# Optimization experiments

Hardware: AMD Instinct MI355X
Metric: run time of the kernel (lower is better)

## Reference

```python
import jax, jax.numpy as jnp
import numpy as np

N = 100_000   # nodes
E = 1_600_000 # edges (avg degree 16)
D = 128       # feature dim (input = hidden = output = mlp hidden)
L = 3         # GIN layers
EPS = 0.0     # init_eps, not learned


def setup_inputs() -> dict:
    key = jax.random.key(0)
    ks = jax.random.split(key, 7)
    feat = jax.random.normal(ks[0], (N, D), jnp.float32)
    # scale weights ~ 1/sqrt(fan_in) for numerically sane activations
    W1 = jax.random.normal(ks[1], (L, D, D), jnp.float32) / np.float32(np.sqrt(D))
    b1 = jax.random.normal(ks[2], (L, D), jnp.float32) * 0.01
    W2 = jax.random.normal(ks[3], (L, D, D), jnp.float32) / np.float32(np.sqrt(D))
    b2 = jax.random.normal(ks[4], (L, D), jnp.float32) * 0.01
    src = jax.random.randint(ks[5], (E,), 0, N, dtype=jnp.int32)
    dst = jax.random.randint(ks[6], (E,), 0, N, dtype=jnp.int32)
    return {"feat": feat, "W1": W1, "b1": b1, "W2": W2, "b2": b2,
            "src": src, "dst": dst}


def reference(feat, W1, b1, W2, b2, src, dst):
    h = feat
    for i in range(L):
        # sum-aggregate neighbor (source) features into destination nodes
        neigh = jax.ops.segment_sum(h[src], dst, num_segments=N)  # [N, D]
        rst = (1.0 + EPS) * h + neigh
        # 2-layer MLP: hidden layer uses act+norm(none), last layer is plain linear
        if i < L - 1:
            h1 = jax.nn.relu(rst @ W1[i] + b1[i])
            h2 = h1 @ W2[i] + b2[i]
            h = jax.nn.relu(h2)  # ApplyNodeFunc: norm(none) -> relu
        else:
            # last GIN layer: activation 'none' everywhere
            h1 = rst @ W1[i] + b1[i]
            h = h1 @ W2[i] + b2[i]
    return h
```

## Files before the change

kernel.cpp:

```cpp
#include <hip/hip_runtime.h>
#include <hip/hip_bf16.h>

#define D 128
#define NBUCK_SHIFT 9
#define PAD_SLACK 2048

typedef __bf16 bf16x8 __attribute__((ext_vector_type(8)));
typedef float f32x4 __attribute__((ext_vector_type(4)));
typedef float f32x2 __attribute__((ext_vector_type(2)));
typedef int i32x4 __attribute__((ext_vector_type(4)));
typedef int i32x2 __attribute__((ext_vector_type(2)));
typedef unsigned int u32x4 __attribute__((ext_vector_type(4)));
typedef unsigned short u16x4_t __attribute__((ext_vector_type(4)));
typedef unsigned short u16x8_t __attribute__((ext_vector_type(8)));

__device__ __forceinline__ unsigned short f2b(float f) {
    __hip_bfloat16 h = __float2bfloat16(f);
    return __builtin_bit_cast(unsigned short, h);
}

__device__ __forceinline__ void acc8(f32x2* acc, u32x4 x) {
#pragma unroll
    for (int r = 0; r < 4; ++r) {
        f32x2 t;
        t[0] = __builtin_bit_cast(float, x[r] << 16);
        t[1] = __builtin_bit_cast(float, x[r] & 0xffff0000u);
        acc[r] += t;
    }
}

__global__ __launch_bounds__(256) void coarse_hist_kernel(
        const int* __restrict__ dst, int* __restrict__ bco, int E, int nbuck) {
    __shared__ int s[256];
    int t = threadIdx.x;
    s[t] = 0;
    __syncthreads();
    for (int i = blockIdx.x * 256 + t; i < E; i += gridDim.x * 256)
        atomicAdd(&s[dst[i] >> NBUCK_SHIFT], 1);
    __syncthreads();
    if (t < nbuck && s[t] > 0) atomicAdd(&bco[t], s[t]);
}

__global__ __launch_bounds__(256) void bucket_scan_kernel(
        const int* __restrict__ bco, int* __restrict__ bbase, int nbuck, int E) {
    __shared__ int s[256];
    int t = threadIdx.x;
    int c = (t < nbuck) ? bco[t] : 0;
    s[t] = c;
    __syncthreads();
    for (int o = 1; o < 256; o <<= 1) {
        int y = (t >= o) ? s[t - o] : 0;
        __syncthreads();
        s[t] += y;
        __syncthreads();
    }
    if (t < nbuck) bbase[t] = s[t] - c;
    if (t == 0) bbase[nbuck] = E;
}

__global__ __launch_bounds__(256) void bucket_kernel(
        const int* __restrict__ src, const int* __restrict__ dst,
        const int* __restrict__ bbase, int* __restrict__ bcursor,
        unsigned int* __restrict__ pairs, int E, int nbuck) {
    __shared__ int lcnt[256];
    __shared__ int lbase[256];
    int t = threadIdx.x;
    int base = blockIdx.x * 4096;
    if (t < nbuck) lcnt[t] = 0;
    __syncthreads();
    int d[16], s[16];
#pragma unroll
    for (int k = 0; k < 16; ++k) {
        int i = base + t + k * 256;
        if (i < E) {
            d[k] = dst[i];
            s[k] = src[i];
            atomicAdd(&lcnt[d[k] >> NBUCK_SHIFT], 1);
        } else {
            d[k] = -1;
            s[k] = 0;
        }
    }
    __syncthreads();
    if (t < nbuck) {
        int c = lcnt[t];
        int g = (c > 0) ? atomicAdd(&bcursor[t], c) : 0;
        lbase[t] = bbase[t] + g;
        lcnt[t] = 0;
    }
    __syncthreads();
#pragma unroll
    for (int k = 0; k < 16; ++k) {
        if (d[k] >= 0) {
            int b = d[k] >> NBUCK_SHIFT;
            int r = atomicAdd(&lcnt[b], 1);
            pairs[lbase[b] + r] = ((unsigned)s[k] << 9) | ((unsigned)d[k] & 511u);
        }
    }
}

__global__ __launch_bounds__(1024) void bucket_build_kernel(
        const unsigned int* __restrict__ pairs, const int* __restrict__ bbase,
        i32x2* __restrict__ rowse, int* __restrict__ col, int* __restrict__ rowhead,
        int N, int E) {
    __shared__ int cnt[512];
    __shared__ int off[512];
    int t = threadIdx.x;
    int b = blockIdx.x;
    int s0 = bbase[b], s1 = bbase[b + 1];
    int p0 = ((s0 + 3) & ~3) + b * PAD_SLACK;
    if (t < 512) cnt[t] = 0;
    __syncthreads();
    for (int i = s0 + t; i < s1; i += 1024)
        atomicAdd(&cnt[pairs[i] & 511u], 1);
    __syncthreads();
    int deg = (t < 512) ? cnt[t] : 0;
    int ovp = (deg > 15) ? ((deg - 15 + 3) & ~3) : 0;
    if (t < 512) off[t] = ovp;
    __syncthreads();
    for (int o = 1; o < 512; o <<= 1) {
        int y = (t < 512 && t >= o) ? off[t - o] : 0;
        __syncthreads();
        if (t < 512) off[t] += y;
        __syncthreads();
    }
    int v0 = b << NBUCK_SHIFT;
    int zoff = N << 8;
    if (t < 512) {
        int ex = off[t] - ovp;
        off[t] = ex;
        cnt[t] = 0;
        int v = v0 + t;
        if (v < N) {
            i32x2 se;
            se[0] = p0 + ex;
            se[1] = p0 + ex + ovp;
            rowse[v] = se;
            int* rhv = rowhead + (size_t)v * 16;
            rhv[0] = v << 8;
            int ninl = deg < 15 ? deg : 15;
            for (int q = 1 + ninl; q < 16; ++q) rhv[q] = zoff;
        }
    }
    __syncthreads();
    for (int i = s0 + t; i < s1; i += 1024) {
        unsigned int p = pairs[i];
        int li = (int)(p & 511u);
        int x = (int)(p >> 9);
        int s = atomicAdd(&cnt[li], 1);
        if (s < 15) rowhead[(size_t)(v0 + li) * 16 + 1 + s] = x << 8;
        else        col[p0 + off[li] + (s - 15)] = x << 8;
    }
    __syncthreads();
    if (t < 512) {
        int cc = cnt[t];
        int ovreal = (cc > 15) ? cc - 15 : 0;
        int base2 = p0 + off[t];
        int endp = base2 + ((ovreal + 3) & ~3);
        for (int q = base2 + ovreal; q < endp; ++q) col[q] = zoff;
    }
}

__global__ void f32_to_bf16_kernel(const float4* __restrict__ in, ushort4* __restrict__ out, int n4) {
    int i = blockIdx.x * blockDim.x + threadIdx.x;
    if (i < n4) {
        float4 f = in[i];
        ushort4 o;
        o.x = f2b(f.x); o.y = f2b(f.y); o.z = f2b(f.z); o.w = f2b(f.w);
        out[i] = o;
    }
}

__global__ void wtrans_kernel(const float* __restrict__ W1, const float* __restrict__ W2,
                              unsigned short* __restrict__ W1L, unsigned short* __restrict__ W2L,
                              int total) {
    int i = blockIdx.x * blockDim.x + threadIdx.x;
    if (i < total) {
        int l = i >> 14;
        int rem = i & 16383;
        int k = rem >> 7;
        int n = rem & 127;
        int nt = n >> 4, l15 = n & 15;
        int kb = k >> 5, lg = (k >> 3) & 3, j = k & 7;
        int o = ((l * 32 + nt * 4 + kb) * 64 + lg * 16 + l15) * 8 + j;
        W1L[o] = f2b(W1[i]);
        W2L[o] = f2b(W2[i]);
    }
}

__global__ __launch_bounds__(256) void agg_kernel(
        const unsigned short* __restrict__ h, const i32x2* __restrict__ rowse,
        const int* __restrict__ col, const i32x4* __restrict__ rowhead,
        unsigned short* __restrict__ rst, int N) {
    int lane = threadIdx.x & 63;
    int i = lane & 15;
    int j = lane >> 4;
    int v = blockIdx.x * 4 + (threadIdx.x >> 6);
    if (v >= N) return;

    const char* __restrict__ hb = (const char*)h;
    unsigned ioff = (unsigned)i * 16u;

    i32x4 c4 = __builtin_nontemporal_load(&rowhead[(size_t)v * 4 + j]);
    i32x2 se = __builtin_nontemporal_load(&rowse[v]);

    f32x2 accA[4], accB[4], accC[4], accD[4];
#pragma unroll
    for (int r = 0; r < 4; ++r) {
        accA[r] = (f32x2){0.f, 0.f};
        accB[r] = (f32x2){0.f, 0.f};
        accC[r] = (f32x2){0.f, 0.f};
        accD[r] = (f32x2){0.f, 0.f};
    }

    u32x4 x0 = *(const u32x4*)(hb + ((unsigned)c4[0] + ioff));
    u32x4 x1 = *(const u32x4*)(hb + ((unsigned)c4[1] + ioff));
    u32x4 x2 = *(const u32x4*)(hb + ((unsigned)c4[2] + ioff));
    u32x4 x3 = *(const u32x4*)(hb + ((unsigned)c4[3] + ioff));

    int e = se[0] + 4 * j;
    int e1 = se[1];
    bool have = (e < e1);
    i32x4 o4;
    if (have) o4 = __builtin_nontemporal_load((const i32x4*)(col + e));

    acc8(accA, x0);
    acc8(accB, x1);
    acc8(accC, x2);
    acc8(accD, x3);

    while (have) {
        int en = e + 16;
        bool haven = (en < e1);
        i32x4 o4n;
        if (haven) o4n = __builtin_nontemporal_load((const i32x4*)(col + en));
        u32x4 y0 = *(const u32x4*)(hb + ((unsigned)o4[0] + ioff));
        u32x4 y1 = *(const u32x4*)(hb + ((unsigned)o4[1] + ioff));
        u32x4 y2 = *(const u32x4*)(hb + ((unsigned)o4[2] + ioff));
        u32x4 y3 = *(const u32x4*)(hb + ((unsigned)o4[3] + ioff));
        acc8(accA, y0);
        acc8(accB, y1);
        acc8(accC, y2);
        acc8(accD, y3);
        o4 = o4n;
        e = en;
        have = haven;
    }

    unsigned short outv[8];
#pragma unroll
    for (int r = 0; r < 4; ++r) {
        f32x2 s = (accA[r] + accB[r]) + (accC[r] + accD[r]);
        float lo = s[0], hi = s[1];
        lo += __shfl_xor(lo, 16);
        lo += __shfl_xor(lo, 32);
        hi += __shfl_xor(hi, 16);
        hi += __shfl_xor(hi, 32);
        outv[2 * r] = f2b(lo);
        outv[2 * r + 1] = f2b(hi);
    }
    if (j == 0) {
        u16x8_t o;
#pragma unroll
        for (int r = 0; r < 8; ++r) o[r] = outv[r];
        *(u16x8_t*)(rst + (size_t)v * D + i * 8) = o;
    }
}

__global__ __launch_bounds__(256, 4) void mlp_kernel(
        const unsigned short* __restrict__ A, const unsigned short* __restrict__ W1L,
        const unsigned short* __restrict__ W2L, const float* __restrict__ b1,
        const float* __restrict__ b2, unsigned short* __restrict__ hOut,
        float* __restrict__ fOut, int mode, int ntiles, int N) {
    __shared__ float b1s[128], b2s[128];
    __shared__ unsigned short tilebuf[4 * 2560];
    int tid = threadIdx.x;
    if (tid < 128) b1s[tid] = b1[tid];
    else b2s[tid - 128] = b2[tid - 128];
    __syncthreads();
    int wave = tid >> 6, lane = tid & 63, l15 = lane & 15, lg = lane >> 4;
    unsigned short* buf = tilebuf + wave * 2560;
    int tile = blockIdx.x * 4 + wave;
    if (tile >= ntiles) return;
    int v0 = tile << 4;

    bf16x8 bfrag[4];
    const unsigned short* arow = A + (size_t)(v0 + l15) * D + lg * 8;
#pragma unroll
    for (int kb = 0; kb < 4; ++kb) bfrag[kb] = *(const bf16x8*)(arow + kb * 32);

    f32x4 acc[8];
#pragma unroll
    for (int nt = 0; nt < 8; ++nt) acc[nt] = (f32x4){0.f, 0.f, 0.f, 0.f};
#pragma unroll
    for (int kb = 0; kb < 4; ++kb)
#pragma unroll
        for (int nt = 0; nt < 8; ++nt) {
            bf16x8 wf = *(const bf16x8*)(W1L + ((nt * 4 + kb) * 64 + lane) * 8);
            acc[nt] = __builtin_amdgcn_mfma_f32_16x16x32_bf16(wf, bfrag[kb], acc[nt], 0, 0, 0);
        }
#pragma unroll
    for (int nt = 0; nt < 8; ++nt) {
        f32x4 bias = *(const f32x4*)(b1s + nt * 16 + lg * 4);
        int kb2 = nt >> 1;
        int lgk = (nt & 1) * 2 + (lg >> 1);
        int U = kb2 * 80 + l15 * 5 + lgk;
        u16x4_t o;
#pragma unroll
        for (int r = 0; r < 4; ++r) {
            float x = acc[nt][r] + bias[r];
            if (mode == 0) x = fmaxf(x, 0.f);
            o[r] = f2b(x);
        }
        *(u16x4_t*)(buf + U * 8 + (lg & 1) * 4) = o;
    }
    bf16x8 bf2[4];
#pragma unroll
    for (int kb = 0; kb < 4; ++kb)
        bf2[kb] = *(const bf16x8*)(buf + (kb * 80 + l15 * 5 + lg) * 8);
#pragma unroll
    for (int nt = 0; nt < 8; ++nt) acc[nt] = (f32x4){0.f, 0.f, 0.f, 0.f};
#pragma unroll
    for (int kb = 0; kb < 4; ++kb)
#pragma unroll
        for (int nt = 0; nt < 8; ++nt) {
            bf16x8 wf = *(const bf16x8*)(W2L + ((nt * 4 + kb) * 64 + lane) * 8);
            acc[nt] = __builtin_amdgcn_mfma_f32_16x16x32_bf16(wf, bf2[kb], acc[nt], 0, 0, 0);
        }
    int m = v0 + l15;
    if (m < N) {
#pragma unroll
        for (int nt = 0; nt < 8; ++nt) {
            f32x4 bias = *(const f32x4*)(b2s + nt * 16 + lg * 4);
            int c0 = nt * 16 + lg * 4;
            if (mode == 0) {
                u16x4_t o;
#pragma unroll
                for (int r = 0; r < 4; ++r) o[r] = f2b(fmaxf(acc[nt][r] + bias[r], 0.f));
                *(u16x4_t*)(hOut + (size_t)m * D + c0) = o;
            } else {
                f32x4 o;
#pragma unroll
                for (int r = 0; r < 4; ++r) o[r] = acc[nt][r] + bias[r];
                *(f32x4*)(fOut + (size_t)m * D + c0) = o;
            }
        }
    }
}

extern "C" void kernel_launch(void* const* d_in, const int* in_sizes, int n_in,
                              void* d_out, int out_size, void* d_ws, size_t ws_size,
                              hipStream_t stream) {
    const float* feat = (const float*)d_in[0];
    const float* W1 = (const float*)d_in[1];
    const float* b1 = (const float*)d_in[2];
    const float* W2 = (const float*)d_in[3];
    const float* b2 = (const float*)d_in[4];
    const int* src = (const int*)d_in[5];
    const int* dst = (const int*)d_in[6];

    const int N = in_sizes[0] / D;
    const int L = in_sizes[2] / D;
    const int E = in_sizes[5];

    char* w = (char*)d_ws;
    size_t off = 0;
    auto alloc = [&](size_t bytes) {
        void* p = w + off;
        off = (off + bytes + 255) & ~(size_t)255;
        return p;
    };
    unsigned short* bufA = (unsigned short*)alloc((size_t)(N + 1) * D * 2);
    unsigned short* bufB = (unsigned short*)alloc((size_t)(N + 1) * D * 2);
    size_t unionBytes = (size_t)(N + 16) * D * 2;
    if ((size_t)E * 4 > unionBytes) unionBytes = (size_t)E * 4;
    unsigned short* bufR = (unsigned short*)alloc(unionBytes);
    unsigned int* pairs = (unsigned int*)bufR;
    int* col = (int*)alloc(((size_t)E + 256 * PAD_SLACK + 16) * 4);
    int* rowhead = (int*)alloc((size_t)N * 16 * 4);
    i32x2* rowse = (i32x2*)alloc((size_t)N * 8);
    int* bco = (int*)alloc(512 * 4);
    int* bcursor = bco + 256;
    int* bbase = (int*)alloc(257 * 4);
    unsigned short* W1L = (unsigned short*)alloc((size_t)L * 16384 * 2);
    unsigned short* W2L = (unsigned short*)alloc((size_t)L * 16384 * 2);

    int nbuck = (N + (1 << NBUCK_SHIFT) - 1) >> NBUCK_SHIFT;

    hipMemsetAsync(bco, 0, 512 * 4, stream);
    hipMemsetAsync(bufA + (size_t)N * D, 0, D * 2, stream);
    hipMemsetAsync(bufB + (size_t)N * D, 0, D * 2, stream);
    coarse_hist_kernel<<<512, 256, 0, stream>>>(dst, bco, E, nbuck);
    bucket_scan_kernel<<<1, 256, 0, stream>>>(bco, bbase, nbuck, E);
    bucket_kernel<<<(E + 4095) / 4096, 256, 0, stream>>>(src, dst, bbase, bcursor, pairs, E, nbuck);
    bucket_build_kernel<<<nbuck, 1024, 0, stream>>>(pairs, bbase, rowse, col, rowhead, N, E);

    int n4 = N * D / 4;
    f32_to_bf16_kernel<<<(n4 + 255) / 256, 256, 0, stream>>>((const float4*)feat, (ushort4*)bufA, n4);
    int wtotal = L * D * D;
    wtrans_kernel<<<(wtotal + 255) / 256, 256, 0, stream>>>(W1, W2, W1L, W2L, wtotal);

    int ntiles = (N + 15) / 16;
    int aggBlocks = (N + 3) / 4;
    int mlpGrid = (ntiles + 3) / 4;
    const unsigned short* hin[3] = {bufA, bufB, bufA};
    unsigned short* hout[3] = {bufB, bufA, nullptr};
    for (int i = 0; i < L; ++i) {
        int mode = (i == L - 1) ? 1 : 0;
        agg_kernel<<<aggBlocks, 256, 0, stream>>>(hin[i], rowse, col, (const i32x4*)rowhead, bufR, N);
        mlp_kernel<<<mlpGrid, 256, 0, stream>>>(bufR, W1L + (size_t)i * 16384, W2L + (size_t)i * 16384,
                                                b1 + i * D, b2 + i * D, hout[i], (float*)d_out,
                                                mode, ntiles, N);
    }
}
```

Baseline: 436.0 us.

## Fuse neighbor aggregation and MLP into one kernel per GIN layer

Replaces the separate aggregation and MLP kernels with one fused kernel per layer. Each block gathers neighbor sums for a 16-node tile into shared memory, then its four waves split the 128 output columns and run both MFMA GEMMs, exchanging the hidden activations through shared memory. This removes the global write and read of the intermediate rst buffer and one launch per layer. In exchange it adds block-wide barriers and lets gather latency and MFMA work serialize inside a block, with 4 nodes per wave processed one after another.

```diff
diff --git a/kernel.cpp b/kernel.cpp
--- a/kernel.cpp
+++ b/kernel.cpp
@@ -188,119 +188,115 @@
     }
 }
 
-__global__ __launch_bounds__(256) void agg_kernel(
+#define RSTRIDE 136
+__global__ __launch_bounds__(256, 4) void fused_kernel(
         const unsigned short* __restrict__ h, const i32x2* __restrict__ rowse,
         const int* __restrict__ col, const i32x4* __restrict__ rowhead,
-        unsigned short* __restrict__ rst, int N) {
-    int lane = threadIdx.x & 63;
-    int i = lane & 15;
-    int j = lane >> 4;
-    int v = blockIdx.x * 4 + (threadIdx.x >> 6);
-    if (v >= N) return;
-
-    const char* __restrict__ hb = (const char*)h;
-    unsigned ioff = (unsigned)i * 16u;
-
-    i32x4 c4 = __builtin_nontemporal_load(&rowhead[(size_t)v * 4 + j]);
-    i32x2 se = __builtin_nontemporal_load(&rowse[v]);
-
-    f32x2 accA[4], accB[4], accC[4], accD[4];
-#pragma unroll
-    for (int r = 0; r < 4; ++r) {
-        accA[r] = (f32x2){0.f, 0.f};
-        accB[r] = (f32x2){0.f, 0.f};
-        accC[r] = (f32x2){0.f, 0.f};
-        accD[r] = (f32x2){0.f, 0.f};
-    }
-
-    u32x4 x0 = *(const u32x4*)(hb + ((unsigned)c4[0] + ioff));
-    u32x4 x1 = *(const u32x4*)(hb + ((unsigned)c4[1] + ioff));
-    u32x4 x2 = *(const u32x4*)(hb + ((unsigned)c4[2] + ioff));
-    u32x4 x3 = *(const u32x4*)(hb + ((unsigned)c4[3] + ioff));
-
-    int e = se[0] + 4 * j;
-    int e1 = se[1];
-    bool have = (e < e1);
-    i32x4 o4;
-    if (have) o4 = __builtin_nontemporal_load((const i32x4*)(col + e));
-
-    acc8(accA, x0);
-    acc8(accB, x1);
-    acc8(accC, x2);
-    acc8(accD, x3);
-
-    while (have) {
-        int en = e + 16;
-        bool haven = (en < e1);
-        i32x4 o4n;
-        if (haven) o4n = __builtin_nontemporal_load((const i32x4*)(col + en));
-        u32x4 y0 = *(const u32x4*)(hb + ((unsigned)o4[0] + ioff));
-        u32x4 y1 = *(const u32x4*)(hb + ((unsigned)o4[1] + ioff));
-        u32x4 y2 = *(const u32x4*)(hb + ((unsigned)o4[2] + ioff));
-        u32x4 y3 = *(const u32x4*)(hb + ((unsigned)o4[3] + ioff));
-        acc8(accA, y0);
-        acc8(accB, y1);
-        acc8(accC, y2);
-        acc8(accD, y3);
-        o4 = o4n;
-        e = en;
-        have = haven;
-    }
-
-    unsigned short outv[8];
-#pragma unroll
-    for (int r = 0; r < 4; ++r) {
-        f32x2 s = (accA[r] + accB[r]) + (accC[r] + accD[r]);
-        float lo = s[0], hi = s[1];
-        lo += __shfl_xor(lo, 16);
-        lo += __shfl_xor(lo, 32);
-        hi += __shfl_xor(hi, 16);
-        hi += __shfl_xor(hi, 32);
-        outv[2 * r] = f2b(lo);
-        outv[2 * r + 1] = f2b(hi);
-    }
-    if (j == 0) {
-        u16x8_t o;
-#pragma unroll
-        for (int r = 0; r < 8; ++r) o[r] = outv[r];
-        *(u16x8_t*)(rst + (size_t)v * D + i * 8) = o;
-    }
-}
-
-__global__ __launch_bounds__(256, 4) void mlp_kernel(
-        const unsigned short* __restrict__ A, const unsigned short* __restrict__ W1L,
-        const unsigned short* __restrict__ W2L, const float* __restrict__ b1,
-        const float* __restrict__ b2, unsigned short* __restrict__ hOut,
-        float* __restrict__ fOut, int mode, int ntiles, int N) {
+        const unsigned short* __restrict__ W1L, const unsigned short* __restrict__ W2L,
+        const float* __restrict__ b1, const float* __restrict__ b2,
+        unsigned short* __restrict__ hOut, float* __restrict__ fOut,
+        int mode, int ntiles, int N) {
     __shared__ float b1s[128], b2s[128];
-    __shared__ unsigned short tilebuf[4 * 2560];
+    __shared__ unsigned short rstile[16 * RSTRIDE];
+    __shared__ unsigned short h1buf[2560];
     int tid = threadIdx.x;
     if (tid < 128) b1s[tid] = b1[tid];
     else b2s[tid - 128] = b2[tid - 128];
-    __syncthreads();
-    int wave = tid >> 6, lane = tid & 63, l15 = lane & 15, lg = lane >> 4;
-    unsigned short* buf = tilebuf + wave * 2560;
-    int tile = blockIdx.x * 4 + wave;
-    if (tile >= ntiles) return;
-    int v0 = tile << 4;
-
+    int wave = tid >> 6, lane = tid & 63;
+    int v0 = blockIdx.x << 4;
+
+    {
+        int i = lane & 15;
+        int j = lane >> 4;
+        const char* __restrict__ hb = (const char*)h;
+        unsigned ioff = (unsigned)i * 16u;
+        for (int q = 0; q < 4; ++q) {
+            int m = wave * 4 + q;
+            int v = v0 + m;
+            f32x2 accA[4], accB[4], accC[4], accD[4];
+#pragma unroll
+            for (int r = 0; r < 4; ++r) {
+                accA[r] = (f32x2){0.f, 0.f};
+                accB[r] = (f32x2){0.f, 0.f};
+                accC[r] = (f32x2){0.f, 0.f};
+                accD[r] = (f32x2){0.f, 0.f};
+            }
+            if (v < N) {
+                i32x4 c4 = __builtin_nontemporal_load(&rowhead[(size_t)v * 4 + j]);
+                i32x2 se = __builtin_nontemporal_load(&rowse[v]);
+                u32x4 x0 = *(const u32x4*)(hb + ((unsigned)c4[0] + ioff));
+                u32x4 x1 = *(const u32x4*)(hb + ((unsigned)c4[1] + ioff));
+                u32x4 x2 = *(const u32x4*)(hb + ((unsigned)c4[2] + ioff));
+                u32x4 x3 = *(const u32x4*)(hb + ((unsigned)c4[3] + ioff));
+                int e = se[0] + 4 * j;
+                int e1 = se[1];
+                bool have = (e < e1);
+                i32x4 o4;
+                if (have) o4 = __builtin_nontemporal_load((const i32x4*)(col + e));
+                acc8(accA, x0);
+                acc8(accB, x1);
+                acc8(accC, x2);
+                acc8(accD, x3);
+                while (have) {
+                    int en = e + 16;
+                    bool haven = (en < e1);
+                    i32x4 o4n;
+                    if (haven) o4n = __builtin_nontemporal_load((const i32x4*)(col + en));
+                    u32x4 y0 = *(const u32x4*)(hb + ((unsigned)o4[0] + ioff));
+                    u32x4 y1 = *(const u32x4*)(hb + ((unsigned)o4[1] + ioff));
+                    u32x4 y2 = *(const u32x4*)(hb + ((unsigned)o4[2] + ioff));
+                    u32x4 y3 = *(const u32x4*)(hb + ((unsigned)o4[3] + ioff));
+                    acc8(accA, y0);
+                    acc8(accB, y1);
+                    acc8(accC, y2);
+                    acc8(accD, y3);
+                    o4 = o4n;
+                    e = en;
+                    have = haven;
+                }
+            }
+            unsigned short outv[8];
+#pragma unroll
+            for (int r = 0; r < 4; ++r) {
+                f32x2 s = (accA[r] + accB[r]) + (accC[r] + accD[r]);
+                float lo = s[0], hi = s[1];
+                lo += __shfl_xor(lo, 16);
+                lo += __shfl_xor(lo, 32);
+                hi += __shfl_xor(hi, 16);
+                hi += __shfl_xor(hi, 32);
+                outv[2 * r] = f2b(lo);
+                outv[2 * r + 1] = f2b(hi);
+            }
+            if (j == 0) {
+                u16x8_t o;
+#pragma unroll
+                for (int r = 0; r < 8; ++r) o[r] = outv[r];
+                *(u16x8_t*)(rstile + m * RSTRIDE + i * 8) = o;
+            }
+        }
+    }
+    __syncthreads();
+
+    int l15 = lane & 15, lg = lane >> 4;
     bf16x8 bfrag[4];
-    const unsigned short* arow = A + (size_t)(v0 + l15) * D + lg * 8;
-#pragma unroll
-    for (int kb = 0; kb < 4; ++kb) bfrag[kb] = *(const bf16x8*)(arow + kb * 32);
-
-    f32x4 acc[8];
-#pragma unroll
-    for (int nt = 0; nt < 8; ++nt) acc[nt] = (f32x4){0.f, 0.f, 0.f, 0.f};
 #pragma unroll
     for (int kb = 0; kb < 4; ++kb)
-#pragma unroll
-        for (int nt = 0; nt < 8; ++nt) {
+        bfrag[kb] = *(const bf16x8*)(rstile + l15 * RSTRIDE + lg * 8 + kb * 32);
+
+    f32x4 acc[2];
+#pragma unroll
+    for (int t = 0; t < 2; ++t) acc[t] = (f32x4){0.f, 0.f, 0.f, 0.f};
+#pragma unroll
+    for (int kb = 0; kb < 4; ++kb)
+#pragma unroll
+        for (int t = 0; t < 2; ++t) {
+            int nt = wave * 2 + t;
             bf16x8 wf = *(const bf16x8*)(W1L + ((nt * 4 + kb) * 64 + lane) * 8);
-            acc[nt] = __builtin_amdgcn_mfma_f32_16x16x32_bf16(wf, bfrag[kb], acc[nt], 0, 0, 0);
-        }
-#pragma unroll
-    for (int nt = 0; nt < 8; ++nt) {
+            acc[t] = __builtin_amdgcn_mfma_f32_16x16x32_bf16(wf, bfrag[kb], acc[t], 0, 0, 0);
+        }
+#pragma unroll
+    for (int t = 0; t < 2; ++t) {
+        int nt = wave * 2 + t;
         f32x4 bias = *(const f32x4*)(b1s + nt * 16 + lg * 4);
         int kb2 = nt >> 1;
         int lgk = (nt & 1) * 2 + (lg >> 1);
@@ -308,40 +304,43 @@
         u16x4_t o;
 #pragma unroll
         for (int r = 0; r < 4; ++r) {
-            float x = acc[nt][r] + bias[r];
+            float x = acc[t][r] + bias[r];
             if (mode == 0) x = fmaxf(x, 0.f);
             o[r] = f2b(x);
         }
-        *(u16x4_t*)(buf + U * 8 + (lg & 1) * 4) = o;
-    }
+        *(u16x4_t*)(h1buf + U * 8 + (lg & 1) * 4) = o;
+    }
+    __syncthreads();
     bf16x8 bf2[4];
 #pragma unroll
     for (int kb = 0; kb < 4; ++kb)
-        bf2[kb] = *(const bf16x8*)(buf + (kb * 80 + l15 * 5 + lg) * 8);
-#pragma unroll
-    for (int nt = 0; nt < 8; ++nt) acc[nt] = (f32x4){0.f, 0.f, 0.f, 0.f};
+        bf2[kb] = *(const bf16x8*)(h1buf + (kb * 80 + l15 * 5 + lg) * 8);
+#pragma unroll
+    for (int t = 0; t < 2; ++t) acc[t] = (f32x4){0.f, 0.f, 0.f, 0.f};
 #pragma unroll
     for (int kb = 0; kb < 4; ++kb)
 #pragma unroll
-        for (int nt = 0; nt < 8; ++nt) {
+        for (int t = 0; t < 2; ++t) {
+            int nt = wave * 2 + t;
             bf16x8 wf = *(const bf16x8*)(W2L + ((nt * 4 + kb) * 64 + lane) * 8);
-            acc[nt] = __builtin_amdgcn_mfma_f32_16x16x32_bf16(wf, bf2[kb], acc[nt], 0, 0, 0);
+            acc[t] = __builtin_amdgcn_mfma_f32_16x16x32_bf16(wf, bf2[kb], acc[t], 0, 0, 0);
         }
     int m = v0 + l15;
     if (m < N) {
 #pragma unroll
-        for (int nt = 0; nt < 8; ++nt) {
+        for (int t = 0; t < 2; ++t) {
+            int nt = wave * 2 + t;
             f32x4 bias = *(const f32x4*)(b2s + nt * 16 + lg * 4);
             int c0 = nt * 16 + lg * 4;
             if (mode == 0) {
                 u16x4_t o;
 #pragma unroll
-                for (int r = 0; r < 4; ++r) o[r] = f2b(fmaxf(acc[nt][r] + bias[r], 0.f));
+                for (int r = 0; r < 4; ++r) o[r] = f2b(fmaxf(acc[t][r] + bias[r], 0.f));
                 *(u16x4_t*)(hOut + (size_t)m * D + c0) = o;
             } else {
                 f32x4 o;
 #pragma unroll
-                for (int r = 0; r < 4; ++r) o[r] = acc[nt][r] + bias[r];
+                for (int r = 0; r < 4; ++r) o[r] = acc[t][r] + bias[r];
                 *(f32x4*)(fOut + (size_t)m * D + c0) = o;
             }
         }
@@ -372,10 +371,7 @@
     };
     unsigned short* bufA = (unsigned short*)alloc((size_t)(N + 1) * D * 2);
     unsigned short* bufB = (unsigned short*)alloc((size_t)(N + 1) * D * 2);
-    size_t unionBytes = (size_t)(N + 16) * D * 2;
-    if ((size_t)E * 4 > unionBytes) unionBytes = (size_t)E * 4;
-    unsigned short* bufR = (unsigned short*)alloc(unionBytes);
-    unsigned int* pairs = (unsigned int*)bufR;
+    unsigned int* pairs = (unsigned int*)alloc((size_t)E * 4);
     int* col = (int*)alloc(((size_t)E + 256 * PAD_SLACK + 16) * 4);
     int* rowhead = (int*)alloc((size_t)N * 16 * 4);
     i32x2* rowse = (i32x2*)alloc((size_t)N * 8);
@@ -401,15 +397,13 @@
     wtrans_kernel<<<(wtotal + 255) / 256, 256, 0, stream>>>(W1, W2, W1L, W2L, wtotal);
 
     int ntiles = (N + 15) / 16;
-    int aggBlocks = (N + 3) / 4;
-    int mlpGrid = (ntiles + 3) / 4;
     const unsigned short* hin[3] = {bufA, bufB, bufA};
     unsigned short* hout[3] = {bufB, bufA, nullptr};
     for (int i = 0; i < L; ++i) {
         int mode = (i == L - 1) ? 1 : 0;
-        agg_kernel<<<aggBlocks, 256, 0, stream>>>(hin[i], rowse, col, (const i32x4*)rowhead, bufR, N);
-        mlp_kernel<<<mlpGrid, 256, 0, stream>>>(bufR, W1L + (size_t)i * 16384, W2L + (size_t)i * 16384,
-                                                b1 + i * D, b2 + i * D, hout[i], (float*)d_out,
-                                                mode, ntiles, N);
-    }
-}
+        fused_kernel<<<ntiles, 256, 0, stream>>>(hin[i], rowse, col, (const i32x4*)rowhead,
+                                                 W1L + (size_t)i * 16384, W2L + (size_t)i * 16384,
+                                                 b1 + i * D, b2 + i * D, hout[i], (float*)d_out,
+                                                 mode, ntiles, N);
+    }
+}
```

After: 397.8 us. 1.1x faster.
